# Kernel optimization log

Hardware: AMD Instinct MI355X
Metric: run time of the kernel (lower is better)

The kernel has to match this reference:

```python
import jax, jax.numpy as jnp
import numpy as np

N_POINTS, N_GRIDS, K = 1024, 512, 7


def setup_inputs() -> dict:
    key = jax.random.key(0)
    k1, k2, k3, k4 = jax.random.split(key, 4)
    points = jax.random.uniform(k1, (N_POINTS, 3), dtype=jnp.float32) * 2.0 - 1.0
    volume_centers = jax.random.uniform(k2, (N_GRIDS, 3), dtype=jnp.float32) * 2.0 - 1.0
    min_s, max_s = 0.01, 1.0
    scales = jax.random.uniform(k3, (N_GRIDS,), dtype=jnp.float32) * (max_s - min_s) + min_s
    mosaic_sdf_values = jax.random.normal(k4, (N_GRIDS, K, K, K), dtype=jnp.float32)
    return {"points": points, "volume_centers": volume_centers,
            "scales": scales, "mosaic_sdf_values": mosaic_sdf_values}


def reference(points, volume_centers, scales, mosaic_sdf_values):
    G, k = mosaic_sdf_values.shape[0], mosaic_sdf_values.shape[1]
    # scaled relative positions: (N, G, 3)
    rel = (points[:, None, :] - volume_centers[None, :, :]) / scales[None, :, None]
    # grid node coordinates in [0,1]^3, flattened: (k^3, 3)
    lin = jnp.linspace(0.0, 1.0, k, dtype=points.dtype)
    gx, gy, gz = jnp.meshgrid(lin, lin, lin, indexing='ij')
    coords = jnp.stack([gx, gy, gz], axis=-1).reshape(-1, 3)
    # squared distance ||rel - coord||^2 expanded -> avoids (N,G,k^3,3) materialization
    d2 = (jnp.sum(rel * rel, axis=-1)[..., None]
          - 2.0 * jnp.einsum('ngd,cd->ngc', rel, coords)
          + jnp.sum(coords * coords, axis=-1)[None, None, :])  # (N, G, k^3)
    dist = jnp.sqrt(jnp.maximum(d2, 0.0))
    # original: weight = dist where dist <= 1 else 0, normalized over grid nodes
    w = jnp.where(dist <= 1.0, dist, 0.0)
    s = jnp.sum(w, axis=-1, keepdims=True)
    w = jnp.where(s > 0, w / jnp.where(s == 0, 1.0, s), 0.0)  # nan_to_num(0) equivalent
    vals = mosaic_sdf_values.reshape(G, -1)  # (G, k^3)
    interp = jnp.einsum('ngc,gc->ng', w, vals)  # (N, G)
    # per-grid blend weight: relu(1 - ||rel||), normalized over grids
    pdist = jnp.linalg.norm(rel, axis=-1)  # (N, G)
    gw = jax.nn.relu(1.0 - pdist)
    gs = jnp.sum(gw, axis=-1, keepdims=True)
    gw = jnp.where(gs > 0, gw / jnp.where(gs == 0, 1.0, gs), 0.0)
    return jnp.sum(interp * gw, axis=-1)  # (N,)
```

## Files before the change

### kernel.cpp

```cpp
#include <hip/hip_runtime.h>


#define NPTS   1024
#define NGRIDS 512
#define STEP   (1.0f / 6.0f)
#define FSQRT(x) __builtin_amdgcn_sqrtf(x)

__global__ __launch_bounds__(128) void msdf_fused(
    const float* __restrict__ points,
    const float* __restrict__ centers,
    const float* __restrict__ scales,
    const float* __restrict__ vals,
    float* __restrict__ out)
{
    __shared__ float  s_v[16 * 343];
    __shared__ float4 s_pair[2][256];
    __shared__ unsigned short s_gid[2][256];
    __shared__ int   s_c[2];
    __shared__ float s_d[2];
    __shared__ float s_a[2];

    const int n    = blockIdx.x;
    const int t    = threadIdx.x;
    const int h    = t >> 6;
    const int lane = t & 63;
    const int grp  = lane >> 3;
    const int sub  = lane & 7;

    float* s_cen = s_v;
    float* s_scl = s_v + 1536;
    {
        const float4* c4 = (const float4*)centers;
        #pragma unroll
        for (int i = 0; i < 3; ++i) ((float4*)s_cen)[t + i * 128] = c4[t + i * 128];
        ((float4*)s_scl)[t] = ((const float4*)scales)[t];
    }
    const float px = points[n * 3 + 0];
    const float py = points[n * 3 + 1];
    const float pz = points[n * 3 + 2];
    __syncthreads();

    float dsum  = 0.0f;
    int   cbase = 0;
    #pragma unroll
    for (int r = 0; r < 4; ++r) {
        const int g = h * 256 + r * 64 + lane;
        const float invs = 1.0f / s_scl[g];
        const float rx = (px - s_cen[g * 3 + 0]) * invs;
        const float ry = (py - s_cen[g * 3 + 1]) * invs;
        const float rz = (pz - s_cen[g * 3 + 2]) * invs;
        const float gwr = 1.0f - FSQRT(rx * rx + ry * ry + rz * rz);
        const bool  act = (gwr > 0.0f);
        const unsigned long long m = __ballot(act);
        if (act) {
            const int pos = cbase + (int)__popcll(m & ((1ull << lane) - 1ull));
            s_pair[h][pos] = make_float4(rx, ry, rz, gwr);
            s_gid[h][pos]  = (unsigned short)g;
            dsum += gwr;
        }
        cbase += (int)__popcll(m);
    }
    #pragma unroll
    for (int off = 32; off >= 1; off >>= 1) dsum += __shfl_xor(dsum, off);
    if (lane == 0) { s_c[h] = cbase; s_d[h] = dsum; }
    __syncthreads();

    const int   c0  = s_c[0];
    const int   C   = c0 + s_c[1];
    const float den = s_d[0] + s_d[1];

    const int base = h * 8 + grp;
    const int nch  = (C > h * 8) ? ((C - h * 8 + 15) >> 4) : 0;
    float* __restrict__ myv = s_v + (h * 8 + grp) * 343;

    float rbuf[43];
    float acc = 0.0f;

    auto issueLoads = [&](int c) {
        const int p  = 16 * c + base;
        const int pc = (p < C) ? p : (C - 1);
        const int ia = (pc < c0) ? 0 : 1;
        const int jp = (pc < c0) ? pc : pc - c0;
        const int gid = (int)s_gid[ia][jp];
        const float* __restrict__ grow = vals + gid * 343;
        #pragma unroll
        for (int k = 0; k < 42; ++k) rbuf[k] = grow[sub + 8 * k];
        rbuf[42] = (sub < 7) ? grow[sub + 336] : 0.0f;
    };

    if (nch > 0) {
        issueLoads(0);
        for (int c = 0; c < nch; ++c) {
            #pragma unroll
            for (int k = 0; k < 42; ++k) myv[sub + 8 * k] = rbuf[k];
            if (sub < 7) myv[sub + 336] = rbuf[42];
            if (c + 1 < nch) issueLoads(c + 1);

            const int p  = 16 * c + base;
            const int pc = (p < C) ? p : (C - 1);
            const int ia = (pc < c0) ? 0 : 1;
            const int jp = (pc < c0) ? pc : pc - c0;
            const float4 pr = s_pair[ia][jp];
            const float  gw = (p < C) ? pr.w : 0.0f;

            float dy2[7], dz2[7];
            #pragma unroll
            for (int j = 0; j < 7; ++j) { const float d = pr.y - j * STEP; dy2[j] = d * d; }
            #pragma unroll
            for (int l = 0; l < 7; ++l) { const float d = pr.z - l * STEP; dz2[l] = d * d; }

            const int   slab = (sub < 7) ? sub : 6;
            const float dxv  = pr.x - slab * STEP;
            const float dx2  = (sub < 7) ? dxv * dxv : 4.0f;
            const float* __restrict__ vrow = myv + slab * 49;

            float ws = 0.0f, vs = 0.0f;
            #pragma unroll
            for (int j = 0; j < 7; ++j) {
                const float dxy = dx2 + dy2[j];
                #pragma unroll
                for (int l = 0; l < 7; ++l) {
                    const float d2 = dxy + dz2[l];
                    const float wt = (d2 <= 1.0f) ? FSQRT(d2) : 0.0f;
                    ws += wt;
                    vs  = fmaf(wt, vrow[j * 7 + l], vs);
                }
            }
            #pragma unroll
            for (int off = 4; off >= 1; off >>= 1) {
                ws += __shfl_xor(ws, off);
                vs += __shfl_xor(vs, off);
            }
            const float interp = (ws > 0.0f) ? (vs / ws) : 0.0f;
            if (sub == 0) acc += interp * gw;
        }
    }

    #pragma unroll
    for (int off = 32; off >= 1; off >>= 1) acc += __shfl_xor(acc, off);
    if (lane == 0) s_a[h] = acc;
    __syncthreads();
    if (t == 0)
        out[n] = (den > 0.0f) ? ((s_a[0] + s_a[1]) / den) : 0.0f;
}

extern "C" void kernel_launch(void* const* d_in, const int* in_sizes, int n_in,
                              void* d_out, int out_size, void* d_ws, size_t ws_size,
                              hipStream_t stream) {
    const float* points  = (const float*)d_in[0];
    const float* centers = (const float*)d_in[1];
    const float* scales  = (const float*)d_in[2];
    const float* vals    = (const float*)d_in[3];
    float* out = (float*)d_out;

    msdf_fused<<<NPTS, 128, 0, stream>>>(points, centers, scales, vals, out);
}
```

Measured before the change: 17.03 us.

## Process two points per block and pool their active grids across four waves

Each block now handles two query points with 256 threads. The active (point, grid) pairs of both points go into one shared work list that all 32 eight-thread groups take from, with per-point accumulators. The goal is better load balance across groups, fewer wasted tail iterations, and one centers/scales staging per two points. The cost is more shared memory (32 padded rows), extra segment-lookup logic and fewer blocks, which may lower occupancy.

New measurement: 16.06 us. -5.7%, faster.

```diff
diff --git a/kernel.cpp b/kernel.cpp
--- a/kernel.cpp
+++ b/kernel.cpp
@@ -3,38 +3,46 @@
 
 #define NPTS   1024
 #define NGRIDS 512
+#define TPB    256
+#define NBLK   512
+#define ROWF   344
 #define STEP   (1.0f / 6.0f)
 #define FSQRT(x) __builtin_amdgcn_sqrtf(x)
 
-__global__ __launch_bounds__(128) void msdf_fused(
+__global__ __launch_bounds__(TPB) void msdf_fused(
     const float* __restrict__ points,
     const float* __restrict__ centers,
     const float* __restrict__ scales,
     const float* __restrict__ vals,
     float* __restrict__ out)
 {
-    __shared__ float  s_v[16 * 343];
-    __shared__ float4 s_pair[2][256];
-    __shared__ unsigned short s_gid[2][256];
-    __shared__ int   s_c[2];
-    __shared__ float s_d[2];
-    __shared__ float s_a[2];
+    __shared__ float  s_v[32][ROWF];
+    __shared__ float4 s_pair[4][256];
+    __shared__ unsigned short s_gid[4][256];
+    __shared__ int   s_c[4];
+    __shared__ float s_d[4];
+    __shared__ float s_red[4][2];
 
-    const int n    = blockIdx.x;
+    const int bid  = blockIdx.x;
     const int t    = threadIdx.x;
-    const int h    = t >> 6;
+    const int w    = t >> 6;
     const int lane = t & 63;
-    const int grp  = lane >> 3;
-    const int sub  = lane & 7;
+    const int grp  = t >> 3;
+    const int sub  = t & 7;
 
-    float* s_cen = s_v;
-    float* s_scl = s_v + 1536;
+    float* s_cen = &s_v[0][0];
+    float* s_scl = s_cen + 1536;
     {
+        float4* dst = (float4*)s_cen;
         const float4* c4 = (const float4*)centers;
-        #pragma unroll
-        for (int i = 0; i < 3; ++i) ((float4*)s_cen)[t + i * 128] = c4[t + i * 128];
-        ((float4*)s_scl)[t] = ((const float4*)scales)[t];
+        const float4* s4 = (const float4*)scales;
+        dst[t] = (t < 384) ? c4[t] : s4[t - 384];
+        const int u = t + 256;
+        dst[u] = (u < 384) ? c4[u] : s4[u - 384];
     }
+
+    const int   p  = w >> 1;
+    const int   n  = (bid << 1) + p;
     const float px = points[n * 3 + 0];
     const float py = points[n * 3 + 1];
     const float pz = points[n * 3 + 2];
@@ -44,7 +52,7 @@
     int   cbase = 0;
     #pragma unroll
     for (int r = 0; r < 4; ++r) {
-        const int g = h * 256 + r * 64 + lane;
+        const int g = ((w & 1) << 8) + (r << 6) + lane;
         const float invs = 1.0f / s_scl[g];
         const float rx = (px - s_cen[g * 3 + 0]) * invs;
         const float ry = (py - s_cen[g * 3 + 1]) * invs;
@@ -54,63 +62,67 @@
         const unsigned long long m = __ballot(act);
         if (act) {
             const int pos = cbase + (int)__popcll(m & ((1ull << lane) - 1ull));
-            s_pair[h][pos] = make_float4(rx, ry, rz, gwr);
-            s_gid[h][pos]  = (unsigned short)g;
+            s_pair[w][pos] = make_float4(rx, ry, rz, gwr);
+            s_gid[w][pos]  = (unsigned short)g;
             dsum += gwr;
         }
         cbase += (int)__popcll(m);
     }
     #pragma unroll
-    for (int off = 32; off >= 1; off >>= 1) dsum += __shfl_xor(dsum, off);
-    if (lane == 0) { s_c[h] = cbase; s_d[h] = dsum; }
+    for (int o = 32; o >= 1; o >>= 1) dsum += __shfl_xor(dsum, o);
+    if (lane == 0) { s_c[w] = cbase; s_d[w] = dsum; }
     __syncthreads();
 
-    const int   c0  = s_c[0];
-    const int   C   = c0 + s_c[1];
-    const float den = s_d[0] + s_d[1];
+    const int o1 = s_c[0];
+    const int o2 = o1 + s_c[1];
+    const int o3 = o2 + s_c[2];
+    const int CT = o3 + s_c[3];
+    const float den0 = s_d[0] + s_d[1];
+    const float den1 = s_d[2] + s_d[3];
 
-    const int base = h * 8 + grp;
-    const int nch  = (C > h * 8) ? ((C - h * 8 + 15) >> 4) : 0;
-    float* __restrict__ myv = s_v + (h * 8 + grp) * 343;
+    float acc0 = 0.0f, acc1 = 0.0f;
+    if (CT > 0) {
+        const int nch = (CT + 31) >> 5;
+        float  rbuf[43];
+        float4 pr;
+        int    gid, seg;
 
-    float rbuf[43];
-    float acc = 0.0f;
+        #define FETCH(a_) {                                               \
+            const int pc = ((a_) < CT) ? (a_) : (CT - 1);                 \
+            seg = (pc >= o1) + (pc >= o2) + (pc >= o3);                   \
+            const int b0 = (seg == 0) ? 0 : (seg == 1) ? o1               \
+                         : (seg == 2) ? o2 : o3;                          \
+            pr  = s_pair[seg][pc - b0];                                   \
+            gid = (int)s_gid[seg][pc - b0]; }
 
-    auto issueLoads = [&](int c) {
-        const int p  = 16 * c + base;
-        const int pc = (p < C) ? p : (C - 1);
-        const int ia = (pc < c0) ? 0 : 1;
-        const int jp = (pc < c0) ? pc : pc - c0;
-        const int gid = (int)s_gid[ia][jp];
-        const float* __restrict__ grow = vals + gid * 343;
-        #pragma unroll
-        for (int k = 0; k < 42; ++k) rbuf[k] = grow[sub + 8 * k];
-        rbuf[42] = (sub < 7) ? grow[sub + 336] : 0.0f;
-    };
+        #define LOADROW() {                                               \
+            const float* __restrict__ grow = vals + gid * 343;            \
+            _Pragma("unroll")                                             \
+            for (int k = 0; k < 42; ++k) rbuf[k] = grow[sub + 8 * k];     \
+            rbuf[42] = (sub < 7) ? grow[336 + sub] : 0.0f; }
 
-    if (nch > 0) {
-        issueLoads(0);
+        FETCH(grp); LOADROW();
+        float* __restrict__ myv = &s_v[grp][0];
+
         for (int c = 0; c < nch; ++c) {
             #pragma unroll
             for (int k = 0; k < 42; ++k) myv[sub + 8 * k] = rbuf[k];
-            if (sub < 7) myv[sub + 336] = rbuf[42];
-            if (c + 1 < nch) issueLoads(c + 1);
+            if (sub < 7) myv[336 + sub] = rbuf[42];
 
-            const int p  = 16 * c + base;
-            const int pc = (p < C) ? p : (C - 1);
-            const int ia = (pc < c0) ? 0 : 1;
-            const int jp = (pc < c0) ? pc : pc - c0;
-            const float4 pr = s_pair[ia][jp];
-            const float  gw = (p < C) ? pr.w : 0.0f;
+            const float4 prc  = pr;
+            const int    segc = seg;
+            const float  gw   = (32 * c + grp < CT) ? prc.w : 0.0f;
+
+            if (c + 1 < nch) { FETCH(32 * (c + 1) + grp); LOADROW(); }
 
             float dy2[7], dz2[7];
             #pragma unroll
-            for (int j = 0; j < 7; ++j) { const float d = pr.y - j * STEP; dy2[j] = d * d; }
+            for (int j = 0; j < 7; ++j) { const float d = prc.y - j * STEP; dy2[j] = d * d; }
             #pragma unroll
-            for (int l = 0; l < 7; ++l) { const float d = pr.z - l * STEP; dz2[l] = d * d; }
+            for (int l = 0; l < 7; ++l) { const float d = prc.z - l * STEP; dz2[l] = d * d; }
 
             const int   slab = (sub < 7) ? sub : 6;
-            const float dxv  = pr.x - slab * STEP;
+            const float dxv  = prc.x - slab * STEP;
             const float dx2  = (sub < 7) ? dxv * dxv : 4.0f;
             const float* __restrict__ vrow = myv + slab * 49;
 
@@ -127,21 +139,33 @@
                 }
             }
             #pragma unroll
-            for (int off = 4; off >= 1; off >>= 1) {
-                ws += __shfl_xor(ws, off);
-                vs += __shfl_xor(vs, off);
+            for (int o = 4; o >= 1; o >>= 1) {
+                ws += __shfl_xor(ws, o);
+                vs += __shfl_xor(vs, o);
             }
             const float interp = (ws > 0.0f) ? (vs / ws) : 0.0f;
-            if (sub == 0) acc += interp * gw;
+            if (sub == 0) {
+                const float contrib = interp * gw;
+                if (segc < 2) acc0 += contrib;
+                else          acc1 += contrib;
+            }
         }
+        #undef FETCH
+        #undef LOADROW
     }
 
     #pragma unroll
-    for (int off = 32; off >= 1; off >>= 1) acc += __shfl_xor(acc, off);
-    if (lane == 0) s_a[h] = acc;
+    for (int o = 32; o >= 1; o >>= 1) {
+        acc0 += __shfl_xor(acc0, o);
+        acc1 += __shfl_xor(acc1, o);
+    }
+    if (lane == 0) { s_red[w][0] = acc0; s_red[w][1] = acc1; }
     __syncthreads();
-    if (t == 0)
-        out[n] = (den > 0.0f) ? ((s_a[0] + s_a[1]) / den) : 0.0f;
+    if (t < 2) {
+        const float nm = s_red[0][t] + s_red[1][t] + s_red[2][t] + s_red[3][t];
+        const float dn = (t == 0) ? den0 : den1;
+        out[(bid << 1) + t] = (dn > 0.0f) ? (nm / dn) : 0.0f;
+    }
 }
 
 extern "C" void kernel_launch(void* const* d_in, const int* in_sizes, int n_in,
@@ -153,5 +177,5 @@
     const float* vals    = (const float*)d_in[3];
     float* out = (float*)d_out;
 
-    msdf_fused<<<NPTS, 128, 0, stream>>>(points, centers, scales, vals, out);
+    msdf_fused<<<NBLK, TPB, 0, stream>>>(points, centers, scales, vals, out);
 }
```
